# Kernel tuning notes

Hardware: AMD Instinct MI355X
Metric: run time of the kernel (lower is better)

Reference implementation:

```python
import jax, jax.numpy as jnp
import numpy as np

N_NODES = 100000


def gcn_layer(x, row, col, W, b):
    """PyG GCNConv with add_self_loops=True, normalize=True, edge_weight=1.
    Aggregates messages from row (source) into col (target)."""
    n = x.shape[0]
    xw = x @ W  # [N, out]
    loop = jnp.arange(n, dtype=row.dtype)
    r = jnp.concatenate([row, loop])
    c = jnp.concatenate([col, loop])
    deg = jax.ops.segment_sum(jnp.ones(r.shape[0], dtype=xw.dtype), c, num_segments=n)
    dinv = jnp.where(deg > 0, deg ** -0.5, 0.0)
    norm = dinv[r] * dinv[c]  # [E+N]
    msg = norm[:, None] * xw[r]  # gather + scale
    out = jax.ops.segment_sum(msg, c, num_segments=n)  # scatter-add
    return out + b


def setup_inputs() -> dict:
    key = jax.random.key(0)
    ks = jax.random.split(key, 12)
    E = 1600000
    x = jax.random.normal(ks[0], (N_NODES, 2), dtype=jnp.float32)
    edge_index = jax.random.randint(ks[1], (2, E), 0, N_NODES, dtype=jnp.int64)
    edge_attr = jax.random.normal(ks[2], (E, 2), dtype=jnp.float32)
    def lin(k, fan_in, fan_out):
        bound = 1.0 / np.sqrt(fan_in)
        kw, kb = jax.random.split(k)
        W = jax.random.uniform(kw, (fan_in, fan_out), minval=-bound, maxval=bound, dtype=jnp.float32)
        b = jax.random.uniform(kb, (fan_out,), minval=-bound, maxval=bound, dtype=jnp.float32)
        return W, b
    W1, b1 = lin(ks[3], 2, 64)
    W2, b2 = lin(ks[4], 64, 32)
    Wm1, bm1 = lin(ks[5], 66, 16)
    Wm2, bm2 = lin(ks[6], 16, 1)
    return {"x": x, "edge_index": edge_index, "edge_attr": edge_attr,
            "W1": W1, "b1": b1, "W2": W2, "b2": b2,
            "Wm1": Wm1, "bm1": bm1, "Wm2": Wm2, "bm2": bm2}


def reference(x, edge_index, edge_attr, W1, b1, W2, b2, Wm1, bm1, Wm2, bm2):
    row, col = edge_index[0], edge_index[1]
    h = jax.nn.relu(gcn_layer(x, row, col, W1, b1))   # [N, 64]
    h = jax.nn.relu(gcn_layer(h, row, col, W2, b2))   # [N, 32]
    # gather-concat per edge: [E, 66]
    ef = jnp.concatenate([h[row], h[col], edge_attr], axis=1)
    hmid = jax.nn.relu(ef @ Wm1 + bm1)  # dropout is identity in eval mode
    out = hmid @ Wm2 + bm2              # [E, 1]
    return out.squeeze(-1)
```

## Files before the change

### kernel.cpp

```cpp
#include <hip/hip_runtime.h>
#include <hip/hip_bf16.h>

typedef __hip_bfloat16 bf16;

__device__ __forceinline__ float ldf(const void* p, int fb, size_t i) {
    if (fb) {
        unsigned int u = ((const unsigned short*)p)[i];
        return __uint_as_float(u << 16);
    }
    return ((const float*)p)[i];
}
__device__ __forceinline__ int ldi(const int* p, int fi, size_t i, int n) {
    int v = fi ? p[2 * i] : p[i];
    return ((unsigned)v < (unsigned)n) ? v : 0;
}
__device__ __forceinline__ float bf2f_bits(unsigned short u) {
    return __uint_as_float(((unsigned int)u) << 16);
}
__device__ __forceinline__ float f16b2f(unsigned short u) {
    _Float16 h = __builtin_bit_cast(_Float16, u);
    return (float)h;
}
__device__ __forceinline__ unsigned short f2f16b(float f) {
    _Float16 h = (_Float16)f;
    return __builtin_bit_cast(unsigned short, h);
}

__global__ void k_detect(const void* x, const int* ei, int* flags) {
    int lane = threadIdx.x;
    const unsigned short* u = (const unsigned short*)x;
    float v0 = bf2f_bits(u[2 * lane]);
    float v1 = bf2f_bits(u[2 * lane + 1]);
    unsigned long long m0 = __ballot(!(v0 > -64.f && v0 < 64.f));
    unsigned long long m1 = __ballot(!(v1 > -64.f && v1 < 64.f));
    unsigned long long mz = __ballot(ei[2 * lane + 1] != 0);
    if (lane == 0) {
        int bad = __popcll(m0) + __popcll(m1);
        flags[0] = (bad >= 4) ? 0 : 1;
        flags[1] = (mz == 0) ? 1 : 0;
    }
}

__global__ void k_sentinel(float* out, int nfloats) {
    int i = blockIdx.x * blockDim.x + threadIdx.x;
    if (i < nfloats) out[i] = 1000.0f;
}

__global__ void k_zero(int* counts, int n1) {
    int i = blockIdx.x * blockDim.x + threadIdx.x;
    if (i < n1) counts[i] = 0;
}

__global__ void k_hist(const int* __restrict__ ei, const int* __restrict__ flags,
                       int* counts, int* __restrict__ rank, int E, int n) {
    int t = blockIdx.x * blockDim.x + threadIdx.x;
    int e0 = t * 4;
    if (e0 >= E) return;
    int fi = flags[1];
    if (e0 + 4 <= E) {
        int c0 = ldi(ei, fi, (size_t)E + e0, n);
        int c1 = ldi(ei, fi, (size_t)E + e0 + 1, n);
        int c2 = ldi(ei, fi, (size_t)E + e0 + 2, n);
        int c3 = ldi(ei, fi, (size_t)E + e0 + 3, n);
        int k0 = atomicAdd(&counts[c0], 1);
        int k1 = atomicAdd(&counts[c1], 1);
        int k2 = atomicAdd(&counts[c2], 1);
        int k3 = atomicAdd(&counts[c3], 1);
        rank[e0]     = k0;
        rank[e0 + 1] = k1;
        rank[e0 + 2] = k2;
        rank[e0 + 3] = k3;
    } else {
        for (int e = e0; e < E; ++e)
            rank[e] = atomicAdd(&counts[ldi(ei, fi, (size_t)E + e, n)], 1);
    }
}

__global__ void k_scan1(const int* __restrict__ counts, int* __restrict__ rowptr,
                        int* __restrict__ chsum, float* __restrict__ dinv,
                        const void* __restrict__ x, const int* __restrict__ flags,
                        float2* __restrict__ xd, int n) {
    __shared__ int s[512];
    int t = threadIdx.x, i = blockIdx.x * 512 + t;
    int v = (i < n) ? counts[i] : 0;
    if (i < n) {
        float di = rsqrtf((float)(v + 1));
        dinv[i] = di;
        int fb = flags[0];
        float2 o;
        o.x = di * ldf(x, fb, 2 * (size_t)i);
        o.y = di * ldf(x, fb, 2 * (size_t)i + 1);
        xd[i] = o;
    }
    s[t] = v;
    __syncthreads();
    for (int off = 1; off < 512; off <<= 1) {
        int add = (t >= off) ? s[t - off] : 0;
        __syncthreads();
        s[t] += add;
        __syncthreads();
    }
    if (i < n) rowptr[i] = s[t] - v;
    if (t == 511) chsum[blockIdx.x] = s[511];
}

__global__ void k_scan2(int* chsum, int nch) {
    __shared__ int s[256];
    int t = threadIdx.x;
    int v = (t < nch) ? chsum[t] : 0;
    s[t] = v;
    __syncthreads();
    for (int off = 1; off < 256; off <<= 1) {
        int add = (t >= off) ? s[t - off] : 0;
        __syncthreads();
        s[t] += add;
        __syncthreads();
    }
    if (t < nch) chsum[t] = s[t] - v;
}

__global__ void k_scan3(int* __restrict__ rowptr, const int* __restrict__ chsum,
                        int n, int E) {
    int t = threadIdx.x, i = blockIdx.x * 512 + t;
    if (i < n) rowptr[i] += chsum[blockIdx.x];
    if (blockIdx.x == 0 && t == 0) rowptr[n] = E;
}

__global__ void k_fill(const int* __restrict__ ei, const int* __restrict__ flags,
                       const int* __restrict__ rowptr, const int* __restrict__ rank,
                       int* __restrict__ srcs, int E, int n) {
    int t = blockIdx.x * blockDim.x + threadIdx.x;
    int e0 = t * 4;
    if (e0 >= E) return;
    int fi = flags[1];
    if (e0 + 4 <= E) {
        int r0 = ldi(ei, fi, e0, n),     c0 = ldi(ei, fi, (size_t)E + e0, n);
        int r1 = ldi(ei, fi, e0 + 1, n), c1 = ldi(ei, fi, (size_t)E + e0 + 1, n);
        int r2 = ldi(ei, fi, e0 + 2, n), c2 = ldi(ei, fi, (size_t)E + e0 + 2, n);
        int r3 = ldi(ei, fi, e0 + 3, n), c3 = ldi(ei, fi, (size_t)E + e0 + 3, n);
        int k0 = rank[e0], k1 = rank[e0 + 1], k2 = rank[e0 + 2], k3 = rank[e0 + 3];
        int p0 = rowptr[c0] + k0;
        int p1 = rowptr[c1] + k1;
        int p2 = rowptr[c2] + k2;
        int p3 = rowptr[c3] + k3;
        srcs[p0] = r0;
        srcs[p1] = r1;
        srcs[p2] = r2;
        srcs[p3] = r3;
    } else {
        for (int e = e0; e < E; ++e) {
            int r = ldi(ei, fi, e, n);
            int c = ldi(ei, fi, (size_t)E + e, n);
            srcs[rowptr[c] + rank[e]] = r;
        }
    }
}

__global__ void k_node1(const float2* __restrict__ xd, const int* __restrict__ flags,
                        const float* __restrict__ dinv, const int* __restrict__ rowptr,
                        const int* __restrict__ srcs,
                        const void* __restrict__ W1, const void* __restrict__ b1,
                        const void* __restrict__ W2,
                        unsigned short* __restrict__ y, int n) {
    __shared__ float sW1[128];
    __shared__ float sb1[64];
    __shared__ float sW2[64 * 32];
    int tid = threadIdx.x;
    int fb = flags[0];
    for (int idx = tid; idx < 128; idx += blockDim.x) sW1[idx] = ldf(W1, fb, idx);
    for (int idx = tid; idx < 64; idx += blockDim.x)  sb1[idx] = ldf(b1, fb, idx);
    for (int idx = tid; idx < 64 * 32; idx += blockDim.x) sW2[idx] = ldf(W2, fb, idx);
    __syncthreads();
    int t = blockIdx.x * blockDim.x + tid;
    int i = t >> 5, lane = t & 31;
    if (i >= n) return;
    int start = rowptr[i], end = rowptr[i + 1];
    float di = dinv[i];
    float p0 = 0.f, p1 = 0.f;
    for (int m = start + lane; m < end; m += 32) {
        int r = srcs[m];
        float2 xv = xd[r];
        p0 += xv.x;
        p1 += xv.y;
    }
#pragma unroll
    for (int off = 16; off; off >>= 1) {
        p0 += __shfl_xor(p0, off, 32);
        p1 += __shfl_xor(p1, off, 32);
    }
    float2 xi = xd[i];
    float a0 = di * (p0 + xi.x);
    float a1 = di * (p1 + xi.y);
    int j = lane;
    float s = 0.f;
#pragma unroll 4
    for (int k = 0; k < 64; ++k) {
        float h = fmaxf(fmaf(a0, sW1[k], fmaf(a1, sW1[64 + k], sb1[k])), 0.f);
        s = fmaf(h, sW2[k * 32 + j], s);
    }
    float ys = di * s;
    y[t] = (unsigned short)(__float_as_uint(ys) >> 16);
}

__global__ void k_gather2q(const unsigned short* __restrict__ y, const int* __restrict__ flags,
                           const float* __restrict__ dinv, const int* __restrict__ rowptr,
                           const int* __restrict__ srcs, const void* __restrict__ b2v,
                           const void* __restrict__ Wm1, const void* __restrict__ bm1,
                           unsigned short* __restrict__ q1, unsigned short* __restrict__ q2, int n) {
    __shared__ float sW[64 * 16];
    __shared__ float sb1[16];
    __shared__ float sb2[32];
    int tid = threadIdx.x;
    int fb = flags[0];
    for (int idx = tid; idx < 64 * 16; idx += blockDim.x) sW[idx] = ldf(Wm1, fb, idx);
    if (tid < 16) sb1[tid] = ldf(bm1, fb, tid);
    if (tid >= 16 && tid < 48) sb2[tid - 16] = ldf(b2v, fb, tid - 16);
    __syncthreads();
    int t = blockIdx.x * blockDim.x + tid;
    int i = t >> 5, lane = t & 31;
    if (i >= n) return;
    float di = dinv[i];
    int start = rowptr[i], end = rowptr[i + 1];
    float acc = bf2f_bits(y[i * 32 + lane]);
    for (int base = start; base < end; base += 32) {
        int cnt = end - base; if (cnt > 32) cnt = 32;
        int sl = (lane < cnt) ? srcs[base + lane] : 0;
        int k = 0;
        for (; k + 4 <= cnt; k += 4) {
            int ra = __shfl(sl, k, 32),     rb = __shfl(sl, k + 1, 32);
            int rc = __shfl(sl, k + 2, 32), rd = __shfl(sl, k + 3, 32);
            float wa = bf2f_bits(y[ra * 32 + lane]);
            float wb = bf2f_bits(y[rb * 32 + lane]);
            float wc = bf2f_bits(y[rc * 32 + lane]);
            float wd = bf2f_bits(y[rd * 32 + lane]);
            acc += (wa + wb) + (wc + wd);
        }
        for (; k < cnt; ++k) {
            int rr = __shfl(sl, k, 32);
            acc += bf2f_bits(y[rr * 32 + lane]);
        }
    }
    float v = fmaxf(fmaf(di, acc, sb2[lane]), 0.f);

    int j = lane & 15;
    int half = lane >> 4;
    float q = half ? 0.f : sb1[j];
    const float* wbase = sW + half * (32 * 16);
#pragma unroll 8
    for (int k = 0; k < 32; ++k) {
        float h = __shfl(v, k, 32);
        q = fmaf(h, wbase[k * 16 + j], q);
    }
    unsigned short qb = f2f16b(q);
    if (half == 0) q1[i * 16 + j] = qb;
    else           q2[i * 16 + j] = qb;
}

__global__ void k_edge_mlp2(const int* __restrict__ ei, const int* __restrict__ flags,
                            const unsigned short* __restrict__ q1,
                            const unsigned short* __restrict__ q2,
                            const void* __restrict__ ea,
                            const void* __restrict__ Wm1, const void* __restrict__ Wm2,
                            const void* __restrict__ bm2,
                            void* __restrict__ out, int E, int n) {
    __shared__ __align__(16) float sWa[16];
    __shared__ __align__(16) float sWb[16];
    __shared__ __align__(16) float sW2[16];
    __shared__ float sB2;
    int tid = threadIdx.x;
    int fb = flags[0], fi = flags[1];
    if (tid < 16) sWa[tid] = ldf(Wm1, fb, 64 * 16 + tid);
    else if (tid < 32) sWb[tid - 16] = ldf(Wm1, fb, 65 * 16 + (tid - 16));
    else if (tid < 48) sW2[tid - 32] = ldf(Wm2, fb, tid - 32);
    else if (tid == 48) sB2 = ldf(bm2, fb, 0);
    __syncthreads();

    int e = blockIdx.x * blockDim.x + tid;
    if (e >= E) return;
    int r = ldi(ei, fi, e, n);
    int c = ldi(ei, fi, (size_t)E + e, n);
    float ea0 = ldf(ea, fb, 2 * (size_t)e), ea1 = ldf(ea, fb, 2 * (size_t)e + 1);

    const uint4* q1u = (const uint4*)q1;
    const uint4* q2u = (const uint4*)q2;
    uint4 A0 = q1u[r * 2], A1 = q1u[r * 2 + 1];
    uint4 B0 = q2u[c * 2], B1 = q2u[c * 2 + 1];

    float o = sB2;
#define E2(uA, uB, JA, JB)                                                          \
    {                                                                               \
        float h0 = f16b2f((unsigned short)((uA) & 0xffffu))                         \
                 + f16b2f((unsigned short)((uB) & 0xffffu))                         \
                 + ea0 * sWa[JA] + ea1 * sWb[JA];                                   \
        o = fmaf(fmaxf(h0, 0.f), sW2[JA], o);                                       \
        float h1 = f16b2f((unsigned short)((uA) >> 16))                             \
                 + f16b2f((unsigned short)((uB) >> 16))                             \
                 + ea0 * sWa[JB] + ea1 * sWb[JB];                                   \
        o = fmaf(fmaxf(h1, 0.f), sW2[JB], o);                                       \
    }
    E2(A0.x, B0.x, 0, 1)   E2(A0.y, B0.y, 2, 3)
    E2(A0.z, B0.z, 4, 5)   E2(A0.w, B0.w, 6, 7)
    E2(A1.x, B1.x, 8, 9)   E2(A1.y, B1.y, 10, 11)
    E2(A1.z, B1.z, 12, 13) E2(A1.w, B1.w, 14, 15)
#undef E2

    if (fb) ((bf16*)out)[e] = __float2bfloat16(o);
    else    ((float*)out)[e] = o;
}

extern "C" void kernel_launch(void* const* d_in, const int* in_sizes, int n_in,
                              void* d_out, int out_size, void* d_ws, size_t ws_size,
                              hipStream_t stream) {
    const void* x   = d_in[0];
    const int*  ei  = (const int*)d_in[1];
    const void* ea  = d_in[2];
    const void* W1  = d_in[3];
    const void* b1  = d_in[4];
    const void* W2  = d_in[5];
    const void* b2  = d_in[6];
    const void* Wm1 = d_in[7];
    const void* bm1 = d_in[8];
    const void* Wm2 = d_in[9];
    const void* bm2 = d_in[10];

    int n = in_sizes[0] / 2;
    int E = in_sizes[2] / 2;

    char* ws = (char*)d_ws;
    size_t off = 0;
    auto take = [&](size_t bytes) -> char* {
        char* p = ws + off;
        off += bytes;
        off = (off + 255) & ~(size_t)255;
        return p;
    };
    int* flags   = (int*)take(8);
    int* counts  = (int*)take((size_t)(n + 1) * 4);
    float* dinv  = (float*)take((size_t)n * 4);
    float2* xd   = (float2*)take((size_t)n * 8);
    int* rowptr  = (int*)take((size_t)(n + 1) * 4);
    int* chsum   = (int*)take(1024);
    int* srcs    = (int*)take((size_t)E * 4);
    unsigned short* y = (unsigned short*)take((size_t)n * 32 * 2);
    size_t qbytes = (size_t)n * 16 * 2;
    size_t ubytes = (size_t)E * 4;
    if (ubytes < 2 * qbytes) ubytes = 2 * qbytes;
    char* un = take(ubytes);
    int* rank = (int*)un;
    unsigned short* q1 = (unsigned short*)un;
    unsigned short* q2 = (unsigned short*)(un + qbytes);

    if (off > ws_size) {
        int nf = out_size / 2;
        if (nf > 0) k_sentinel<<<(nf + 255) / 256, 256, 0, stream>>>((float*)d_out, nf);
        return;
    }

    const int B = 256;
    int nch = (n + 511) / 512;
    int E4 = (E + 3) / 4;
    k_detect<<<1, 64, 0, stream>>>(x, ei, flags);
    k_zero<<<(n + 1 + B - 1) / B, B, 0, stream>>>(counts, n + 1);
    k_hist<<<(E4 + B - 1) / B, B, 0, stream>>>(ei, flags, counts, rank, E, n);
    k_scan1<<<nch, 512, 0, stream>>>(counts, rowptr, chsum, dinv, x, flags, xd, n);
    k_scan2<<<1, 256, 0, stream>>>(chsum, nch);
    k_scan3<<<nch, 512, 0, stream>>>(rowptr, chsum, n, E);
    k_fill<<<(E4 + B - 1) / B, B, 0, stream>>>(ei, flags, rowptr, rank, srcs, E, n);
    k_node1<<<((size_t)n * 32 + B - 1) / B, B, 0, stream>>>(xd, flags, dinv, rowptr, srcs,
                                                            W1, b1, W2, y, n);
    k_gather2q<<<((size_t)n * 32 + B - 1) / B, B, 0, stream>>>(y, flags, dinv, rowptr, srcs,
                                                               b2, Wm1, bm1, q1, q2, n);
    k_edge_mlp2<<<(E + B - 1) / B, B, 0, stream>>>(ei, flags, q1, q2, ea, Wm1, Wm2, bm2,
                                                   d_out, E, n);
}
```

Baseline: 324.6 us.

## Fuse small launches, vectorize edge index loads, widen per-thread work across kernels

Merges the detect and zero kernels into one, and folds the chunk-sum scan into the rowptr fixup kernel so each block redoes the small scan. Histogram and fill now handle 8 edges per thread using int4 loads and stores. The gather loop is unrolled to 8 neighbours, and the edge MLP processes two edges per thread. counts and srcs now share one buffer. This cuts launch count and raises memory-level parallelism, at the cost of redundant scan work per block and more register pressure.

```diff
diff --git a/kernel.cpp b/kernel.cpp
--- a/kernel.cpp
+++ b/kernel.cpp
@@ -14,6 +14,9 @@
     int v = fi ? p[2 * i] : p[i];
     return ((unsigned)v < (unsigned)n) ? v : 0;
 }
+__device__ __forceinline__ int clampn(int v, int n) {
+    return ((unsigned)v < (unsigned)n) ? v : 0;
+}
 __device__ __forceinline__ float bf2f_bits(unsigned short u) {
     return __uint_as_float(((unsigned int)u) << 16);
 }
@@ -26,18 +29,22 @@
     return __builtin_bit_cast(unsigned short, h);
 }
 
-__global__ void k_detect(const void* x, const int* ei, int* flags) {
-    int lane = threadIdx.x;
-    const unsigned short* u = (const unsigned short*)x;
-    float v0 = bf2f_bits(u[2 * lane]);
-    float v1 = bf2f_bits(u[2 * lane + 1]);
-    unsigned long long m0 = __ballot(!(v0 > -64.f && v0 < 64.f));
-    unsigned long long m1 = __ballot(!(v1 > -64.f && v1 < 64.f));
-    unsigned long long mz = __ballot(ei[2 * lane + 1] != 0);
-    if (lane == 0) {
-        int bad = __popcll(m0) + __popcll(m1);
-        flags[0] = (bad >= 4) ? 0 : 1;
-        flags[1] = (mz == 0) ? 1 : 0;
+__global__ void k_dz(const void* x, const int* ei, int* flags, int* counts, int n1) {
+    int i = blockIdx.x * blockDim.x + threadIdx.x;
+    if (i < n1) counts[i] = 0;
+    if (blockIdx.x == 0 && threadIdx.x < 64) {
+        int lane = threadIdx.x;
+        const unsigned short* u = (const unsigned short*)x;
+        float v0 = bf2f_bits(u[2 * lane]);
+        float v1 = bf2f_bits(u[2 * lane + 1]);
+        unsigned long long m0 = __ballot(!(v0 > -64.f && v0 < 64.f));
+        unsigned long long m1 = __ballot(!(v1 > -64.f && v1 < 64.f));
+        unsigned long long mz = __ballot(ei[2 * lane + 1] != 0);
+        if (lane == 0) {
+            int bad = __popcll(m0) + __popcll(m1);
+            flags[0] = (bad >= 4) ? 0 : 1;
+            flags[1] = (mz == 0) ? 1 : 0;
+        }
     }
 }
 
@@ -46,30 +53,38 @@
     if (i < nfloats) out[i] = 1000.0f;
 }
 
-__global__ void k_zero(int* counts, int n1) {
-    int i = blockIdx.x * blockDim.x + threadIdx.x;
-    if (i < n1) counts[i] = 0;
-}
-
 __global__ void k_hist(const int* __restrict__ ei, const int* __restrict__ flags,
                        int* counts, int* __restrict__ rank, int E, int n) {
     int t = blockIdx.x * blockDim.x + threadIdx.x;
-    int e0 = t * 4;
+    int e0 = t * 8;
     if (e0 >= E) return;
     int fi = flags[1];
-    if (e0 + 4 <= E) {
-        int c0 = ldi(ei, fi, (size_t)E + e0, n);
-        int c1 = ldi(ei, fi, (size_t)E + e0 + 1, n);
-        int c2 = ldi(ei, fi, (size_t)E + e0 + 2, n);
-        int c3 = ldi(ei, fi, (size_t)E + e0 + 3, n);
+    if (e0 + 8 <= E) {
+        int c0, c1, c2, c3, c4, c5, c6, c7;
+        if (fi) {
+            const int4* p = (const int4*)(ei + 2 * ((size_t)E + e0));
+            int4 a = p[0], b = p[1], c = p[2], d = p[3];
+            c0 = a.x; c1 = a.z; c2 = b.x; c3 = b.z;
+            c4 = c.x; c5 = c.z; c6 = d.x; c7 = d.z;
+        } else {
+            const int4* p = (const int4*)(ei + (size_t)E + e0);
+            int4 a = p[0], b = p[1];
+            c0 = a.x; c1 = a.y; c2 = a.z; c3 = a.w;
+            c4 = b.x; c5 = b.y; c6 = b.z; c7 = b.w;
+        }
+        c0 = clampn(c0, n); c1 = clampn(c1, n); c2 = clampn(c2, n); c3 = clampn(c3, n);
+        c4 = clampn(c4, n); c5 = clampn(c5, n); c6 = clampn(c6, n); c7 = clampn(c7, n);
         int k0 = atomicAdd(&counts[c0], 1);
         int k1 = atomicAdd(&counts[c1], 1);
         int k2 = atomicAdd(&counts[c2], 1);
         int k3 = atomicAdd(&counts[c3], 1);
-        rank[e0]     = k0;
-        rank[e0 + 1] = k1;
-        rank[e0 + 2] = k2;
-        rank[e0 + 3] = k3;
+        int k4 = atomicAdd(&counts[c4], 1);
+        int k5 = atomicAdd(&counts[c5], 1);
+        int k6 = atomicAdd(&counts[c6], 1);
+        int k7 = atomicAdd(&counts[c7], 1);
+        int4* rp = (int4*)(rank + e0);
+        rp[0] = make_int4(k0, k1, k2, k3);
+        rp[1] = make_int4(k4, k5, k6, k7);
     } else {
         for (int e = e0; e < E; ++e)
             rank[e] = atomicAdd(&counts[ldi(ei, fi, (size_t)E + e, n)], 1);
@@ -104,25 +119,27 @@
     if (t == 511) chsum[blockIdx.x] = s[511];
 }
 
-__global__ void k_scan2(int* chsum, int nch) {
+__global__ void k_scan3(int* __restrict__ rowptr, const int* __restrict__ chsum,
+                        int nch, int n, int E) {
     __shared__ int s[256];
+    __shared__ int boff;
     int t = threadIdx.x;
-    int v = (t < nch) ? chsum[t] : 0;
-    s[t] = v;
+    if (t < 256) s[t] = (t < nch) ? chsum[t] : 0;
     __syncthreads();
     for (int off = 1; off < 256; off <<= 1) {
-        int add = (t >= off) ? s[t - off] : 0;
+        int add = 0;
+        if (t < 256 && t >= off) add = s[t - off];
         __syncthreads();
-        s[t] += add;
+        if (t < 256) s[t] += add;
         __syncthreads();
     }
-    if (t < nch) chsum[t] = s[t] - v;
-}
-
-__global__ void k_scan3(int* __restrict__ rowptr, const int* __restrict__ chsum,
-                        int n, int E) {
-    int t = threadIdx.x, i = blockIdx.x * 512 + t;
-    if (i < n) rowptr[i] += chsum[blockIdx.x];
+    if (t == 0) {
+        int own = (blockIdx.x < (unsigned)nch) ? chsum[blockIdx.x] : 0;
+        boff = s[blockIdx.x] - own;
+    }
+    __syncthreads();
+    int i = blockIdx.x * 512 + t;
+    if (i < n) rowptr[i] += boff;
     if (blockIdx.x == 0 && t == 0) rowptr[n] = E;
 }
 
@@ -130,23 +147,45 @@
                        const int* __restrict__ rowptr, const int* __restrict__ rank,
                        int* __restrict__ srcs, int E, int n) {
     int t = blockIdx.x * blockDim.x + threadIdx.x;
-    int e0 = t * 4;
+    int e0 = t * 8;
     if (e0 >= E) return;
     int fi = flags[1];
-    if (e0 + 4 <= E) {
-        int r0 = ldi(ei, fi, e0, n),     c0 = ldi(ei, fi, (size_t)E + e0, n);
-        int r1 = ldi(ei, fi, e0 + 1, n), c1 = ldi(ei, fi, (size_t)E + e0 + 1, n);
-        int r2 = ldi(ei, fi, e0 + 2, n), c2 = ldi(ei, fi, (size_t)E + e0 + 2, n);
-        int r3 = ldi(ei, fi, e0 + 3, n), c3 = ldi(ei, fi, (size_t)E + e0 + 3, n);
-        int k0 = rank[e0], k1 = rank[e0 + 1], k2 = rank[e0 + 2], k3 = rank[e0 + 3];
-        int p0 = rowptr[c0] + k0;
-        int p1 = rowptr[c1] + k1;
-        int p2 = rowptr[c2] + k2;
-        int p3 = rowptr[c3] + k3;
-        srcs[p0] = r0;
-        srcs[p1] = r1;
-        srcs[p2] = r2;
-        srcs[p3] = r3;
+    if (e0 + 8 <= E) {
+        int r0, r1, r2, r3, r4, r5, r6, r7;
+        int c0, c1, c2, c3, c4, c5, c6, c7;
+        if (fi) {
+            const int4* pr = (const int4*)(ei + 2 * (size_t)e0);
+            int4 a = pr[0], b = pr[1], c = pr[2], d = pr[3];
+            r0 = a.x; r1 = a.z; r2 = b.x; r3 = b.z;
+            r4 = c.x; r5 = c.z; r6 = d.x; r7 = d.z;
+            const int4* pc = (const int4*)(ei + 2 * ((size_t)E + e0));
+            a = pc[0]; b = pc[1]; c = pc[2]; d = pc[3];
+            c0 = a.x; c1 = a.z; c2 = b.x; c3 = b.z;
+            c4 = c.x; c5 = c.z; c6 = d.x; c7 = d.z;
+        } else {
+            const int4* pr = (const int4*)(ei + (size_t)e0);
+            int4 a = pr[0], b = pr[1];
+            r0 = a.x; r1 = a.y; r2 = a.z; r3 = a.w;
+            r4 = b.x; r5 = b.y; r6 = b.z; r7 = b.w;
+            const int4* pc = (const int4*)(ei + (size_t)E + e0);
+            a = pc[0]; b = pc[1];
+            c0 = a.x; c1 = a.y; c2 = a.z; c3 = a.w;
+            c4 = b.x; c5 = b.y; c6 = b.z; c7 = b.w;
+        }
+        r0 = clampn(r0, n); r1 = clampn(r1, n); r2 = clampn(r2, n); r3 = clampn(r3, n);
+        r4 = clampn(r4, n); r5 = clampn(r5, n); r6 = clampn(r6, n); r7 = clampn(r7, n);
+        c0 = clampn(c0, n); c1 = clampn(c1, n); c2 = clampn(c2, n); c3 = clampn(c3, n);
+        c4 = clampn(c4, n); c5 = clampn(c5, n); c6 = clampn(c6, n); c7 = clampn(c7, n);
+        const int4* kp = (const int4*)(rank + e0);
+        int4 ka = kp[0], kb = kp[1];
+        srcs[rowptr[c0] + ka.x] = r0;
+        srcs[rowptr[c1] + ka.y] = r1;
+        srcs[rowptr[c2] + ka.z] = r2;
+        srcs[rowptr[c3] + ka.w] = r3;
+        srcs[rowptr[c4] + kb.x] = r4;
+        srcs[rowptr[c5] + kb.y] = r5;
+        srcs[rowptr[c6] + kb.z] = r6;
+        srcs[rowptr[c7] + kb.w] = r7;
     } else {
         for (int e = e0; e < E; ++e) {
             int r = ldi(ei, fi, e, n);
@@ -226,14 +265,20 @@
         int cnt = end - base; if (cnt > 32) cnt = 32;
         int sl = (lane < cnt) ? srcs[base + lane] : 0;
         int k = 0;
-        for (; k + 4 <= cnt; k += 4) {
-            int ra = __shfl(sl, k, 32),     rb = __shfl(sl, k + 1, 32);
-            int rc = __shfl(sl, k + 2, 32), rd = __shfl(sl, k + 3, 32);
-            float wa = bf2f_bits(y[ra * 32 + lane]);
-            float wb = bf2f_bits(y[rb * 32 + lane]);
-            float wc = bf2f_bits(y[rc * 32 + lane]);
-            float wd = bf2f_bits(y[rd * 32 + lane]);
-            acc += (wa + wb) + (wc + wd);
+        for (; k + 8 <= cnt; k += 8) {
+            int r0 = __shfl(sl, k, 32),     r1 = __shfl(sl, k + 1, 32);
+            int r2 = __shfl(sl, k + 2, 32), r3 = __shfl(sl, k + 3, 32);
+            int r4 = __shfl(sl, k + 4, 32), r5 = __shfl(sl, k + 5, 32);
+            int r6 = __shfl(sl, k + 6, 32), r7 = __shfl(sl, k + 7, 32);
+            float w0 = bf2f_bits(y[r0 * 32 + lane]);
+            float w1 = bf2f_bits(y[r1 * 32 + lane]);
+            float w2 = bf2f_bits(y[r2 * 32 + lane]);
+            float w3 = bf2f_bits(y[r3 * 32 + lane]);
+            float w4 = bf2f_bits(y[r4 * 32 + lane]);
+            float w5 = bf2f_bits(y[r5 * 32 + lane]);
+            float w6 = bf2f_bits(y[r6 * 32 + lane]);
+            float w7 = bf2f_bits(y[r7 * 32 + lane]);
+            acc += ((w0 + w1) + (w2 + w3)) + ((w4 + w5) + (w6 + w7));
         }
         for (; k < cnt; ++k) {
             int rr = __shfl(sl, k, 32);
@@ -255,6 +300,29 @@
     if (half == 0) q1[i * 16 + j] = qb;
     else           q2[i * 16 + j] = qb;
 }
+
+#define EMLP_BODY(A0, A1, B0, B1, EA0, EA1, O)                                      \
+    {                                                                               \
+        float o = sB2;                                                              \
+        float ea0 = (EA0), ea1 = (EA1);                                             \
+        _Pragma("unroll")                                                           \
+        for (int w = 0; w < 8; ++w) {                                               \
+            unsigned int uA = (w < 4) ? ((const unsigned int*)&A0)[w]               \
+                                      : ((const unsigned int*)&A1)[w - 4];          \
+            unsigned int uB = (w < 4) ? ((const unsigned int*)&B0)[w]               \
+                                      : ((const unsigned int*)&B1)[w - 4];          \
+            int JA = 2 * w, JB = 2 * w + 1;                                         \
+            float h0 = f16b2f((unsigned short)(uA & 0xffffu))                       \
+                     + f16b2f((unsigned short)(uB & 0xffffu))                       \
+                     + ea0 * sWa[JA] + ea1 * sWb[JA];                               \
+            o = fmaf(fmaxf(h0, 0.f), sW2[JA], o);                                   \
+            float h1 = f16b2f((unsigned short)(uA >> 16))                           \
+                     + f16b2f((unsigned short)(uB >> 16))                           \
+                     + ea0 * sWa[JB] + ea1 * sWb[JB];                               \
+            o = fmaf(fmaxf(h1, 0.f), sW2[JB], o);                                   \
+        }                                                                           \
+        (O) = o;                                                                    \
+    }
 
 __global__ void k_edge_mlp2(const int* __restrict__ ei, const int* __restrict__ flags,
                             const unsigned short* __restrict__ q1,
@@ -275,38 +343,40 @@
     else if (tid == 48) sB2 = ldf(bm2, fb, 0);
     __syncthreads();
 
-    int e = blockIdx.x * blockDim.x + tid;
-    if (e >= E) return;
-    int r = ldi(ei, fi, e, n);
-    int c = ldi(ei, fi, (size_t)E + e, n);
-    float ea0 = ldf(ea, fb, 2 * (size_t)e), ea1 = ldf(ea, fb, 2 * (size_t)e + 1);
+    int T = (E + 1) >> 1;
+    int t0 = blockIdx.x * blockDim.x + tid;
+    if (t0 >= T) return;
+    int eA = t0, eB = t0 + T;
+    int hasB = (eB < E);
+
+    int rA = ldi(ei, fi, eA, n);
+    int cA = ldi(ei, fi, (size_t)E + eA, n);
+    int rB = hasB ? ldi(ei, fi, eB, n) : 0;
+    int cB = hasB ? ldi(ei, fi, (size_t)E + eB, n) : 0;
+    float eaA0 = ldf(ea, fb, 2 * (size_t)eA), eaA1 = ldf(ea, fb, 2 * (size_t)eA + 1);
+    float eaB0 = hasB ? ldf(ea, fb, 2 * (size_t)eB) : 0.f;
+    float eaB1 = hasB ? ldf(ea, fb, 2 * (size_t)eB + 1) : 0.f;
 
     const uint4* q1u = (const uint4*)q1;
     const uint4* q2u = (const uint4*)q2;
-    uint4 A0 = q1u[r * 2], A1 = q1u[r * 2 + 1];
-    uint4 B0 = q2u[c * 2], B1 = q2u[c * 2 + 1];
-
-    float o = sB2;
-#define E2(uA, uB, JA, JB)                                                          \
-    {                                                                               \
-        float h0 = f16b2f((unsigned short)((uA) & 0xffffu))                         \
-                 + f16b2f((unsigned short)((uB) & 0xffffu))                         \
-                 + ea0 * sWa[JA] + ea1 * sWb[JA];                                   \
-        o = fmaf(fmaxf(h0, 0.f), sW2[JA], o);                                       \
-        float h1 = f16b2f((unsigned short)((uA) >> 16))                             \
-                 + f16b2f((unsigned short)((uB) >> 16))                             \
-                 + ea0 * sWa[JB] + ea1 * sWb[JB];                                   \
-        o = fmaf(fmaxf(h1, 0.f), sW2[JB], o);                                       \
-    }
-    E2(A0.x, B0.x, 0, 1)   E2(A0.y, B0.y, 2, 3)
-    E2(A0.z, B0.z, 4, 5)   E2(A0.w, B0.w, 6, 7)
-    E2(A1.x, B1.x, 8, 9)   E2(A1.y, B1.y, 10, 11)
-    E2(A1.z, B1.z, 12, 13) E2(A1.w, B1.w, 14, 15)
-#undef E2
-
-    if (fb) ((bf16*)out)[e] = __float2bfloat16(o);
-    else    ((float*)out)[e] = o;
-}
+    uint4 A0 = q1u[rA * 2], A1 = q1u[rA * 2 + 1];
+    uint4 B0 = q2u[cA * 2], B1 = q2u[cA * 2 + 1];
+    uint4 C0 = q1u[rB * 2], C1 = q1u[rB * 2 + 1];
+    uint4 D0 = q2u[cB * 2], D1 = q2u[cB * 2 + 1];
+
+    float oA, oB;
+    EMLP_BODY(A0, A1, B0, B1, eaA0, eaA1, oA)
+    EMLP_BODY(C0, C1, D0, D1, eaB0, eaB1, oB)
+
+    if (fb) {
+        ((bf16*)out)[eA] = __float2bfloat16(oA);
+        if (hasB) ((bf16*)out)[eB] = __float2bfloat16(oB);
+    } else {
+        ((float*)out)[eA] = oA;
+        if (hasB) ((float*)out)[eB] = oB;
+    }
+}
+#undef EMLP_BODY
 
 extern "C" void kernel_launch(void* const* d_in, const int* in_sizes, int n_in,
                               void* d_out, int out_size, void* d_ws, size_t ws_size,
@@ -335,20 +405,23 @@
         return p;
     };
     int* flags   = (int*)take(8);
-    int* counts  = (int*)take((size_t)(n + 1) * 4);
     float* dinv  = (float*)take((size_t)n * 4);
     float2* xd   = (float2*)take((size_t)n * 8);
     int* rowptr  = (int*)take((size_t)(n + 1) * 4);
     int* chsum   = (int*)take(1024);
-    int* srcs    = (int*)take((size_t)E * 4);
+    size_t aBytes = (size_t)E * 4;
+    if (aBytes < (size_t)(n + 1) * 4) aBytes = (size_t)(n + 1) * 4;
+    char* ua = take(aBytes);
+    int* counts = (int*)ua;
+    int* srcs   = (int*)ua;
     unsigned short* y = (unsigned short*)take((size_t)n * 32 * 2);
     size_t qbytes = (size_t)n * 16 * 2;
-    size_t ubytes = (size_t)E * 4;
-    if (ubytes < 2 * qbytes) ubytes = 2 * qbytes;
-    char* un = take(ubytes);
-    int* rank = (int*)un;
-    unsigned short* q1 = (unsigned short*)un;
-    unsigned short* q2 = (unsigned short*)(un + qbytes);
+    size_t bBytes = (size_t)E * 4;
+    if (bBytes < 2 * qbytes) bBytes = 2 * qbytes;
+    char* ub = take(bBytes);
+    int* rank = (int*)ub;
+    unsigned short* q1 = (unsigned short*)ub;
+    unsigned short* q2 = (unsigned short*)(ub + qbytes);
 
     if (off > ws_size) {
         int nf = out_size / 2;
@@ -358,18 +431,17 @@
 
     const int B = 256;
     int nch = (n + 511) / 512;
-    int E4 = (E + 3) / 4;
-    k_detect<<<1, 64, 0, stream>>>(x, ei, flags);
-    k_zero<<<(n + 1 + B - 1) / B, B, 0, stream>>>(counts, n + 1);
-    k_hist<<<(E4 + B - 1) / B, B, 0, stream>>>(ei, flags, counts, rank, E, n);
+    int E8 = (E + 7) / 8;
+    k_dz<<<(n + 1 + B - 1) / B, B, 0, stream>>>(x, ei, flags, counts, n + 1);
+    k_hist<<<(E8 + B - 1) / B, B, 0, stream>>>(ei, flags, counts, rank, E, n);
     k_scan1<<<nch, 512, 0, stream>>>(counts, rowptr, chsum, dinv, x, flags, xd, n);
-    k_scan2<<<1, 256, 0, stream>>>(chsum, nch);
-    k_scan3<<<nch, 512, 0, stream>>>(rowptr, chsum, n, E);
-    k_fill<<<(E4 + B - 1) / B, B, 0, stream>>>(ei, flags, rowptr, rank, srcs, E, n);
+    k_scan3<<<nch, 512, 0, stream>>>(rowptr, chsum, nch, n, E);
+    k_fill<<<(E8 + B - 1) / B, B, 0, stream>>>(ei, flags, rowptr, rank, srcs, E, n);
     k_node1<<<((size_t)n * 32 + B - 1) / B, B, 0, stream>>>(xd, flags, dinv, rowptr, srcs,
                                                             W1, b1, W2, y, n);
     k_gather2q<<<((size_t)n * 32 + B - 1) / B, B, 0, stream>>>(y, flags, dinv, rowptr, srcs,
                                                                b2, Wm1, bm1, q1, q2, n);
-    k_edge_mlp2<<<(E + B - 1) / B, B, 0, stream>>>(ei, flags, q1, q2, ea, Wm1, Wm2, bm2,
-                                                   d_out, E, n);
-}
+    int T2 = (E + 1) / 2;
+    k_edge_mlp2<<<(T2 + B - 1) / B, B, 0, stream>>>(ei, flags, q1, q2, ea, Wm1, Wm2, bm2,
+                                                    d_out, E, n);
+}
```

Measured after the change: 331.3 us. 1.02x slower.
